# Kernel optimization log

Hardware: AMD Instinct MI355X
Metric: run time of the kernel (lower is better)

The kernel has to match this reference:

```python
import jax, jax.numpy as jnp
import numpy as np

A0 = 0.5291772105638411
KE = 14.399645351950548


def _softplus_inverse(x):
    return x + np.log(-np.expm1(-x))


def _sigma(x):
    # exp(-1/clamp(x,1e-12)) underflows to 0 for x<=0, so the where is nan-free
    return jnp.where(x > 0, jnp.exp(-1.0 / jnp.maximum(x, 1e-12)), 0.0)


def _switch(x, x_on, x_off):
    c = (x - x_on) / (x_off - x_on)
    s1 = _sigma(1.0 - c)
    s0 = _sigma(c)
    return s1 / (s1 + s0 + 1e-12)


def setup_inputs() -> dict:
    key = jax.random.key(0)
    k0, k1, k2, k3, k4 = jax.random.split(key, 5)
    N = 100000
    E = 6400000
    atomic_numbers = jax.random.uniform(k0, (N,), jnp.float32, 1.0, 30.0)
    cutoffs = jax.random.uniform(k1, (E, 1), jnp.float32)
    lengths = jax.random.uniform(k2, (E, 1), jnp.float32, 0.5, 3.0)
    senders = jax.random.randint(k3, (E,), 0, N)
    receivers = jax.random.randint(k4, (E,), 0, N)
    init = dict(a1=3.2, a2=0.9423, a3=0.4028, a4=0.2016,
                c1=0.1818, c2=0.5099, c3=0.2802, c4=0.02817,
                p=0.23, d=1.0 / (0.8854 * A0))
    params = {k + '_raw': jnp.asarray([_softplus_inverse(v)], jnp.float32)
              for k, v in init.items()}
    out = {'atomic_numbers': atomic_numbers, 'cutoffs': cutoffs,
           'senders': senders, 'receivers': receivers,
           'lengths': lengths, 'num_nodes': N}
    out.update(params)
    return out


def reference(atomic_numbers, cutoffs, senders, receivers, lengths, num_nodes,
              a1_raw, a2_raw, a3_raw, a4_raw,
              c1_raw, c2_raw, c3_raw, c4_raw, p_raw, d_raw):
    sp = jax.nn.softplus
    a1, a2, a3, a4 = sp(a1_raw), sp(a2_raw), sp(a3_raw), sp(a4_raw)
    c1, c2, c3, c4 = sp(c1_raw), sp(c2_raw), sp(c3_raw), sp(c4_raw)
    p, d = sp(p_raw), sp(d_raw)
    c_sum = c1 + c2 + c3 + c4
    c1, c2, c3, c4 = c1 / c_sum, c2 / c_sum, c3 / c_sum, c4 / c_sum

    cut = cutoffs[:, 0]   # [E]
    L = lengths[:, 0]     # [E]
    z_i = atomic_numbers[receivers]
    z_j = atomic_numbers[senders]

    x = KE * cut * (z_i * z_j) / jnp.maximum(L, 1e-6)
    rzd = L * (jnp.power(z_i, p) + jnp.power(z_j, p)) * d
    y = (c1 * jnp.exp(-a1 * rzd) + c2 * jnp.exp(-a2 * rzd)
         + c3 * jnp.exp(-a3 * rzd) + c4 * jnp.exp(-a4 * rzd))
    w = _switch(L, 0.0, 1.5)
    e_rep_edge = w * x * y * 0.5
    return jax.ops.segment_sum(e_rep_edge, receivers, num_segments=num_nodes)[:, None]
```

## Files before the change

kernel.cpp:

```cpp
#include <hip/hip_runtime.h>
#include <math.h>

#define C0KE 7.199822675975274f
#define LOG2E 1.4426950408889634f
#define BSHIFT 8
#define NBK 391
#define SLOTS 16
#define REG (NBK * SLOTS)
#define NBLK 1024
#define K1T 512
#define SENTINEL 0xFFFFFFFFu

__device__ __forceinline__ float softplusf(float x) {
    return (x > 20.0f) ? x : log1pf(__expf(x));
}

struct ZblParams { float A1, A2, A3, A4, c1, c2, c3, c4, p; };

__device__ __forceinline__ void load_params(
    const float* a1r, const float* a2r, const float* a3r, const float* a4r,
    const float* c1r, const float* c2r, const float* c3r, const float* c4r,
    const float* pr, const float* dr, ZblParams* P)
{
    float d  = softplusf(dr[0]);
    float s  = d * LOG2E;
    P->A1 = softplusf(a1r[0]) * s;
    P->A2 = softplusf(a2r[0]) * s;
    P->A3 = softplusf(a3r[0]) * s;
    P->A4 = softplusf(a4r[0]) * s;
    float c1 = softplusf(c1r[0]), c2 = softplusf(c2r[0]);
    float c3 = softplusf(c3r[0]), c4 = softplusf(c4r[0]);
    float inv = 1.0f / (c1 + c2 + c3 + c4);
    P->c1 = c1 * inv; P->c2 = c2 * inv; P->c3 = c3 * inv; P->c4 = c4 * inv;
    P->p = softplusf(pr[0]);
}

__device__ __forceinline__ float edge_energy_fast(
    float l, float cut_, float zi, float zj, const ZblParams& P)
{
    float c  = l * (1.0f / 1.5f);
    float om = 1.0f - c;
    float s1 = __builtin_amdgcn_exp2f(-LOG2E * __builtin_amdgcn_rcpf(om));
    float s0 = __builtin_amdgcn_exp2f(-LOG2E * __builtin_amdgcn_rcpf(c));
    float w  = s1 * __builtin_amdgcn_rcpf(s1 + s0);
    float x  = C0KE * cut_ * zi * zj * __builtin_amdgcn_rcpf(l);
    float S  = __builtin_amdgcn_exp2f(P.p * __builtin_amdgcn_logf(zi))
             + __builtin_amdgcn_exp2f(P.p * __builtin_amdgcn_logf(zj));
    float t  = l * S;
    float y  = P.c1 * __builtin_amdgcn_exp2f(-P.A1 * t)
             + P.c2 * __builtin_amdgcn_exp2f(-P.A2 * t)
             + P.c3 * __builtin_amdgcn_exp2f(-P.A3 * t)
             + P.c4 * __builtin_amdgcn_exp2f(-P.A4 * t);
    return w * x * y;
}

__global__ __launch_bounds__(K1T) void zbl_build(
    const float* __restrict__ z, const float* __restrict__ cut,
    const int* __restrict__ snd, const int* __restrict__ rcv,
    const float* __restrict__ len,
    const float* __restrict__ a1r, const float* __restrict__ a2r,
    const float* __restrict__ a3r, const float* __restrict__ a4r,
    const float* __restrict__ c1r, const float* __restrict__ c2r,
    const float* __restrict__ c3r, const float* __restrict__ c4r,
    const float* __restrict__ pr,  const float* __restrict__ dr,
    unsigned* __restrict__ Pg,
    float* __restrict__ out,
    int EPB, int E)
{
    __shared__ ZblParams P;
    __shared__ unsigned slots[REG];
    __shared__ unsigned fillc[NBK];

    const int tid = threadIdx.x;
    if (tid == 0)
        load_params(a1r, a2r, a3r, a4r, c1r, c2r, c3r, c4r, pr, dr, &P);
    for (int i = tid; i < REG; i += K1T) slots[i] = SENTINEL;
    for (int b = tid; b < NBK; b += K1T) fillc[b] = 0u;
    __syncthreads();
    const ZblParams Pl = P;

    const int blk = blockIdx.x;
    const int e0 = blk * EPB;
    const int e1 = min(e0 + EPB, E);
    const int nv = (e1 > e0) ? ((e1 - e0) >> 2) : 0;
    const int qb = e0 >> 2;
    const int etail = e0 + (nv << 2);
    const float4* Lq = (const float4*)len;
    const int4*   Rq = (const int4*)rcv;
    const float4* Cq = (const float4*)cut;
    const int4*   Sq = (const int4*)snd;

    for (int q = tid; q < nv; q += K1T) {
        float4 l4 = Lq[qb + q];
        if (l4.x < 1.5f || l4.y < 1.5f || l4.z < 1.5f || l4.w < 1.5f) {
            int4   r4 = Rq[qb + q];
            float4 c4 = Cq[qb + q];
            int4   s4 = Sq[qb + q];
            float Ls[4] = {l4.x, l4.y, l4.z, l4.w};
            float Cs[4] = {c4.x, c4.y, c4.z, c4.w};
            int   Ss[4] = {s4.x, s4.y, s4.z, s4.w};
            int   Rs[4] = {r4.x, r4.y, r4.z, r4.w};
            #pragma unroll
            for (int k = 0; k < 4; ++k) {
                if (Ls[k] < 1.5f) {
                    unsigned r = (unsigned)Rs[k];
                    float v = edge_energy_fast(Ls[k], Cs[k],
                                z[r], z[(unsigned)Ss[k]], Pl);
                    unsigned bk = r >> BSHIFT;
                    unsigned tk = atomicAdd(&fillc[bk], 1u);
                    if (tk < SLOTS) {
                        slots[bk * SLOTS + tk] =
                            (__float_as_uint(v) & 0xFFFFFF00u) | (r & 0xFFu);
                    } else {
                        unsafeAtomicAdd(&out[r], v);
                    }
                }
            }
        }
    }
    for (int e = etail + tid; e < e1; e += K1T) {
        float l = len[e];
        if (l < 1.5f) {
            unsigned r = (unsigned)rcv[e];
            float v = edge_energy_fast(l, cut[e], z[r], z[(unsigned)snd[e]], Pl);
            unsigned bk = r >> BSHIFT;
            unsigned tk = atomicAdd(&fillc[bk], 1u);
            if (tk < SLOTS)
                slots[bk * SLOTS + tk] =
                    (__float_as_uint(v) & 0xFFFFFF00u) | (r & 0xFFu);
            else
                unsafeAtomicAdd(&out[r], v);
        }
    }
    __syncthreads();

    unsigned base = (unsigned)blk * (unsigned)REG;
    for (int i = tid; i < REG; i += K1T)
        Pg[base + i] = slots[i];
}

__global__ __launch_bounds__(512) void zbl_reduce(
    const unsigned* __restrict__ Pg, float* __restrict__ out, int N)
{
    __shared__ float acc[256];
    const int tid = threadIdx.x;
    if (tid < 256) acc[tid] = 0.0f;
    __syncthreads();

    const int b = blockIdx.x;
    const uint4* Pq = (const uint4*)Pg;
    const int total = NBLK * (SLOTS / 4);
    for (int lin = tid; lin < total; lin += 512) {
        int r = lin >> 2, q = lin & 3;
        uint4 u = Pq[(size_t)r * (REG / 4) + (size_t)b * (SLOTS / 4) + q];
        if (u.x != SENTINEL)
            atomicAdd(&acc[u.x & 255u], __uint_as_float(u.x & 0xFFFFFF00u));
        if (u.y != SENTINEL)
            atomicAdd(&acc[u.y & 255u], __uint_as_float(u.y & 0xFFFFFF00u));
        if (u.z != SENTINEL)
            atomicAdd(&acc[u.z & 255u], __uint_as_float(u.z & 0xFFFFFF00u));
        if (u.w != SENTINEL)
            atomicAdd(&acc[u.w & 255u], __uint_as_float(u.w & 0xFFFFFF00u));
    }
    __syncthreads();

    int n = (b << BSHIFT) + tid;
    if (tid < 256 && n < N)
        out[n] += acc[tid];
}

__global__ __launch_bounds__(256) void zbl_direct(
    const float* __restrict__ z, const float* __restrict__ cut,
    const int* __restrict__ snd, const int* __restrict__ rcv,
    const float* __restrict__ len,
    const float* __restrict__ a1r, const float* __restrict__ a2r,
    const float* __restrict__ a3r, const float* __restrict__ a4r,
    const float* __restrict__ c1r, const float* __restrict__ c2r,
    const float* __restrict__ c3r, const float* __restrict__ c4r,
    const float* __restrict__ pr,  const float* __restrict__ dr,
    float* __restrict__ out, int n4, int E)
{
    __shared__ ZblParams P;
    if (threadIdx.x == 0)
        load_params(a1r, a2r, a3r, a4r, c1r, c2r, c3r, c4r, pr, dr, &P);
    __syncthreads();
    const ZblParams Pl = P;

    int i = blockIdx.x * blockDim.x + threadIdx.x;
    if (i >= n4) return;
    int base = i * 4;
    float cs[4], Ls[4]; int ss[4], rr[4]; int cnt;
    if (base + 4 <= E) {
        float4 c4v = ((const float4*)cut)[i];
        float4 l4v = ((const float4*)len)[i];
        int4   s4v = ((const int4*)snd)[i];
        int4   r4v = ((const int4*)rcv)[i];
        cs[0]=c4v.x; cs[1]=c4v.y; cs[2]=c4v.z; cs[3]=c4v.w;
        Ls[0]=l4v.x; Ls[1]=l4v.y; Ls[2]=l4v.z; Ls[3]=l4v.w;
        ss[0]=s4v.x; ss[1]=s4v.y; ss[2]=s4v.z; ss[3]=s4v.w;
        rr[0]=r4v.x; rr[1]=r4v.y; rr[2]=r4v.z; rr[3]=r4v.w;
        cnt = 4;
    } else {
        cnt = E - base;
        for (int k = 0; k < cnt; ++k) {
            cs[k] = cut[base+k]; Ls[k] = len[base+k];
            ss[k] = snd[base+k]; rr[k] = rcv[base+k];
        }
    }
    #pragma unroll
    for (int k = 0; k < 4; ++k) {
        if (k >= cnt) break;
        if (Ls[k] < 1.5f) {
            float e_rep = edge_energy_fast(Ls[k], cs[k], z[rr[k]], z[ss[k]], Pl);
            unsafeAtomicAdd(&out[rr[k]], e_rep);
        }
    }
}

extern "C" void kernel_launch(void* const* d_in, const int* in_sizes, int n_in,
                              void* d_out, int out_size, void* d_ws, size_t ws_size,
                              hipStream_t stream) {
    const float* z   = (const float*)d_in[0];
    const float* cut = (const float*)d_in[1];
    const int*   snd = (const int*)d_in[2];
    const int*   rcv = (const int*)d_in[3];
    const float* len = (const float*)d_in[4];
    const float* a1r = (const float*)d_in[6];
    const float* a2r = (const float*)d_in[7];
    const float* a3r = (const float*)d_in[8];
    const float* a4r = (const float*)d_in[9];
    const float* c1r = (const float*)d_in[10];
    const float* c2r = (const float*)d_in[11];
    const float* c3r = (const float*)d_in[12];
    const float* c4r = (const float*)d_in[13];
    const float* pr  = (const float*)d_in[14];
    const float* dr  = (const float*)d_in[15];

    float* out = (float*)d_out;
    int E = in_sizes[2];
    int N = out_size;

    size_t need1 = (size_t)NBLK * REG * sizeof(unsigned);

    hipMemsetAsync(d_out, 0, (size_t)N * sizeof(float), stream);

    if (ws_size >= need1) {
        int EPB = (((E + NBLK - 1) / NBLK) + 3) & ~3;
        unsigned* Pg = (unsigned*)d_ws;
        hipLaunchKernelGGL(zbl_build, dim3(NBLK), dim3(K1T), 0, stream,
                           z, cut, snd, rcv, len,
                           a1r, a2r, a3r, a4r, c1r, c2r, c3r, c4r, pr, dr,
                           Pg, out, EPB, E);
        hipLaunchKernelGGL(zbl_reduce, dim3(NBK), dim3(512), 0, stream,
                           (const unsigned*)Pg, out, N);
    } else {
        int n4 = (E + 3) / 4;
        int blocks = (n4 + 255) / 256;
        hipLaunchKernelGGL(zbl_direct, dim3(blocks), dim3(256), 0, stream,
                           z, cut, snd, rcv, len,
                           a1r, a2r, a3r, a4r, c1r, c2r, c3r, c4r, pr, dr,
                           out, n4, E);
    }
}
```

Before: 205.6 us.

## Prefetch next edge quad, batch z gathers, halve blocks, widen slot buffers

Software-pipelines the edge loop so each thread loads the next float4/int4 quad of lengths, receivers, cutoffs and senders while it processes the current one. It also issues all z gathers for a quad before computing energies, and loads all four arrays unconditionally instead of skipping them when no length passes the cutoff. Block count drops from 1024 to 512 with 20 slots per bucket, which shrinks the partial buffer the reduce kernel scans. Slot initialisation and write-back now use 128-bit vector stores. The trade-offs are more registers, extra bandwidth from the dropped length filter, and fewer blocks for parallelism and latency hiding.

```diff
diff --git a/kernel.cpp b/kernel.cpp
--- a/kernel.cpp
+++ b/kernel.cpp
@@ -5,9 +5,9 @@
 #define LOG2E 1.4426950408889634f
 #define BSHIFT 8
 #define NBK 391
-#define SLOTS 16
+#define SLOTS 20
 #define REG (NBK * SLOTS)
-#define NBLK 1024
+#define NBLK 512
 #define K1T 512
 #define SENTINEL 0xFFFFFFFFu
 
@@ -74,7 +74,11 @@
     const int tid = threadIdx.x;
     if (tid == 0)
         load_params(a1r, a2r, a3r, a4r, c1r, c2r, c3r, c4r, pr, dr, &P);
-    for (int i = tid; i < REG; i += K1T) slots[i] = SENTINEL;
+    {
+        uint4* s4p = (uint4*)slots;
+        const uint4 sent = make_uint4(SENTINEL, SENTINEL, SENTINEL, SENTINEL);
+        for (int i = tid; i < REG / 4; i += K1T) s4p[i] = sent;
+    }
     for (int b = tid; b < NBK; b += K1T) fillc[b] = 0u;
     __syncthreads();
     const ZblParams Pl = P;
@@ -90,22 +94,40 @@
     const float4* Cq = (const float4*)cut;
     const int4*   Sq = (const int4*)snd;
 
-    for (int q = tid; q < nv; q += K1T) {
-        float4 l4 = Lq[qb + q];
-        if (l4.x < 1.5f || l4.y < 1.5f || l4.z < 1.5f || l4.w < 1.5f) {
-            int4   r4 = Rq[qb + q];
-            float4 c4 = Cq[qb + q];
-            int4   s4 = Sq[qb + q];
+    const int trips = (nv + K1T - 1) / K1T;
+    int rel = tid;
+    int qi  = qb + tid;
+    bool have = rel < nv;
+    float4 l4, c4; int4 r4, s4;
+    if (have) { l4 = Lq[qi]; r4 = Rq[qi]; c4 = Cq[qi]; s4 = Sq[qi]; }
+
+    for (int it = 0; it < trips; ++it) {
+        const int reln = rel + K1T;
+        const int qin  = qi + K1T;
+        const bool haveN = reln < nv;
+        float4 l4n, c4n; int4 r4n, s4n;
+        if (haveN) { l4n = Lq[qin]; r4n = Rq[qin]; c4n = Cq[qin]; s4n = Sq[qin]; }
+
+        if (have) {
             float Ls[4] = {l4.x, l4.y, l4.z, l4.w};
             float Cs[4] = {c4.x, c4.y, c4.z, c4.w};
             int   Ss[4] = {s4.x, s4.y, s4.z, s4.w};
             int   Rs[4] = {r4.x, r4.y, r4.z, r4.w};
+            bool  pass[4];
+            float zi[4], zj[4];
             #pragma unroll
             for (int k = 0; k < 4; ++k) {
-                if (Ls[k] < 1.5f) {
-                    unsigned r = (unsigned)Rs[k];
-                    float v = edge_energy_fast(Ls[k], Cs[k],
-                                z[r], z[(unsigned)Ss[k]], Pl);
+                pass[k] = Ls[k] < 1.5f;
+                if (pass[k]) {
+                    zi[k] = z[(unsigned)Rs[k]];
+                    zj[k] = z[(unsigned)Ss[k]];
+                }
+            }
+            #pragma unroll
+            for (int k = 0; k < 4; ++k) {
+                if (pass[k]) {
+                    float v = edge_energy_fast(Ls[k], Cs[k], zi[k], zj[k], Pl);
+                    unsigned r  = (unsigned)Rs[k];
                     unsigned bk = r >> BSHIFT;
                     unsigned tk = atomicAdd(&fillc[bk], 1u);
                     if (tk < SLOTS) {
@@ -117,7 +139,10 @@
                 }
             }
         }
-    }
+        l4 = l4n; c4 = c4n; r4 = r4n; s4 = s4n;
+        rel = reln; qi = qin; have = haveN;
+    }
+
     for (int e = etail + tid; e < e1; e += K1T) {
         float l = len[e];
         if (l < 1.5f) {
@@ -134,9 +159,11 @@
     }
     __syncthreads();
 
-    unsigned base = (unsigned)blk * (unsigned)REG;
-    for (int i = tid; i < REG; i += K1T)
-        Pg[base + i] = slots[i];
+    {
+        uint4* dst = (uint4*)(Pg + (size_t)blk * REG);
+        const uint4* src = (const uint4*)slots;
+        for (int i = tid; i < REG / 4; i += K1T) dst[i] = src[i];
+    }
 }
 
 __global__ __launch_bounds__(512) void zbl_reduce(
@@ -151,7 +178,8 @@
     const uint4* Pq = (const uint4*)Pg;
     const int total = NBLK * (SLOTS / 4);
     for (int lin = tid; lin < total; lin += 512) {
-        int r = lin >> 2, q = lin & 3;
+        int r = lin / (SLOTS / 4);
+        int q = lin - r * (SLOTS / 4);
         uint4 u = Pq[(size_t)r * (REG / 4) + (size_t)b * (SLOTS / 4) + q];
         if (u.x != SENTINEL)
             atomicAdd(&acc[u.x & 255u], __uint_as_float(u.x & 0xFFFFFF00u));
```

Result: faster. 198.2 us (-3.6%).

## Replace shared-memory slot binning with replicated global atomic accumulation arrays

Applied to the files above, without the earlier changes.

Drops the per-block LDS slot-binning build and the reduce pass that scanned every block's slots. Edges now go straight to global atomic adds on one of 16 replicated output arrays, chosen by block index, and a merge kernel then sums the replicas into the output. This removes the large partial-slot workspace writes and the reduce scan, and spreads atomic contention across the replicas. The cost is clearing and reading 16×N floats and more global atomics, because every surviving edge now does one instead of only the overflow edges.

```diff
diff --git a/kernel.cpp b/kernel.cpp
--- a/kernel.cpp
+++ b/kernel.cpp
@@ -3,13 +3,8 @@
 
 #define C0KE 7.199822675975274f
 #define LOG2E 1.4426950408889634f
-#define BSHIFT 8
-#define NBK 391
-#define SLOTS 16
-#define REG (NBK * SLOTS)
-#define NBLK 1024
-#define K1T 512
-#define SENTINEL 0xFFFFFFFFu
+#define RREP 16
+#define SCT 256
 
 __device__ __forceinline__ float softplusf(float x) {
     return (x > 20.0f) ? x : log1pf(__expf(x));
@@ -54,7 +49,7 @@
     return w * x * y;
 }
 
-__global__ __launch_bounds__(K1T) void zbl_build(
+__global__ __launch_bounds__(SCT) void zbl_scatter(
     const float* __restrict__ z, const float* __restrict__ cut,
     const int* __restrict__ snd, const int* __restrict__ rcv,
     const float* __restrict__ len,
@@ -63,110 +58,84 @@
     const float* __restrict__ c1r, const float* __restrict__ c2r,
     const float* __restrict__ c3r, const float* __restrict__ c4r,
     const float* __restrict__ pr,  const float* __restrict__ dr,
-    unsigned* __restrict__ Pg,
-    float* __restrict__ out,
-    int EPB, int E)
+    float* __restrict__ ws,
+    int nq, int E, int N)
 {
     __shared__ ZblParams P;
-    __shared__ unsigned slots[REG];
-    __shared__ unsigned fillc[NBK];
-
-    const int tid = threadIdx.x;
-    if (tid == 0)
+    if (threadIdx.x == 0)
         load_params(a1r, a2r, a3r, a4r, c1r, c2r, c3r, c4r, pr, dr, &P);
-    for (int i = tid; i < REG; i += K1T) slots[i] = SENTINEL;
-    for (int b = tid; b < NBK; b += K1T) fillc[b] = 0u;
     __syncthreads();
     const ZblParams Pl = P;
 
-    const int blk = blockIdx.x;
-    const int e0 = blk * EPB;
-    const int e1 = min(e0 + EPB, E);
-    const int nv = (e1 > e0) ? ((e1 - e0) >> 2) : 0;
-    const int qb = e0 >> 2;
-    const int etail = e0 + (nv << 2);
-    const float4* Lq = (const float4*)len;
-    const int4*   Rq = (const int4*)rcv;
-    const float4* Cq = (const float4*)cut;
-    const int4*   Sq = (const int4*)snd;
-
-    for (int q = tid; q < nv; q += K1T) {
-        float4 l4 = Lq[qb + q];
-        if (l4.x < 1.5f || l4.y < 1.5f || l4.z < 1.5f || l4.w < 1.5f) {
-            int4   r4 = Rq[qb + q];
-            float4 c4 = Cq[qb + q];
-            int4   s4 = Sq[qb + q];
-            float Ls[4] = {l4.x, l4.y, l4.z, l4.w};
-            float Cs[4] = {c4.x, c4.y, c4.z, c4.w};
-            int   Ss[4] = {s4.x, s4.y, s4.z, s4.w};
-            int   Rs[4] = {r4.x, r4.y, r4.z, r4.w};
+    float* __restrict__ rw = ws + (size_t)(blockIdx.x & (RREP - 1)) * (size_t)N;
+
+    int i = blockIdx.x * SCT + threadIdx.x;
+    if (i >= nq) return;
+    int base = i << 2;
+
+    float Ls[4], Cs[4]; int Ss[4], Rs[4]; int cnt;
+    if (base + 4 <= E) {
+        float4 l4 = ((const float4*)len)[i];
+        int4   r4 = ((const int4*)rcv)[i];
+        float4 c4 = ((const float4*)cut)[i];
+        int4   s4 = ((const int4*)snd)[i];
+        Ls[0]=l4.x; Ls[1]=l4.y; Ls[2]=l4.z; Ls[3]=l4.w;
+        Cs[0]=c4.x; Cs[1]=c4.y; Cs[2]=c4.z; Cs[3]=c4.w;
+        Ss[0]=s4.x; Ss[1]=s4.y; Ss[2]=s4.z; Ss[3]=s4.w;
+        Rs[0]=r4.x; Rs[1]=r4.y; Rs[2]=r4.z; Rs[3]=r4.w;
+        cnt = 4;
+    } else {
+        cnt = E - base;
+        for (int k = 0; k < cnt; ++k) {
+            Ls[k] = len[base+k]; Cs[k] = cut[base+k];
+            Ss[k] = snd[base+k]; Rs[k] = rcv[base+k];
+        }
+    }
+
+    bool pass[4]; float zi[4], zj[4];
+    #pragma unroll
+    for (int k = 0; k < 4; ++k) {
+        pass[k] = (k < cnt) && (Ls[k] < 1.5f);
+        if (pass[k]) {
+            zi[k] = z[(unsigned)Rs[k]];
+            zj[k] = z[(unsigned)Ss[k]];
+        }
+    }
+    #pragma unroll
+    for (int k = 0; k < 4; ++k) {
+        if (pass[k]) {
+            float v = edge_energy_fast(Ls[k], Cs[k], zi[k], zj[k], Pl);
+            unsafeAtomicAdd(&rw[(unsigned)Rs[k]], v);
+        }
+    }
+}
+
+__global__ __launch_bounds__(256) void zbl_merge(
+    const float* __restrict__ ws, float* __restrict__ out, int N)
+{
+    const int idx = blockIdx.x * 256 + threadIdx.x;
+    const int stride = gridDim.x * 256;
+    if ((N & 3) == 0) {
+        const int n4 = N >> 2;
+        const float4* w4 = (const float4*)ws;
+        float4* o4 = (float4*)out;
+        for (int i = idx; i < n4; i += stride) {
+            float4 s = w4[i];
             #pragma unroll
-            for (int k = 0; k < 4; ++k) {
-                if (Ls[k] < 1.5f) {
-                    unsigned r = (unsigned)Rs[k];
-                    float v = edge_energy_fast(Ls[k], Cs[k],
-                                z[r], z[(unsigned)Ss[k]], Pl);
-                    unsigned bk = r >> BSHIFT;
-                    unsigned tk = atomicAdd(&fillc[bk], 1u);
-                    if (tk < SLOTS) {
-                        slots[bk * SLOTS + tk] =
-                            (__float_as_uint(v) & 0xFFFFFF00u) | (r & 0xFFu);
-                    } else {
-                        unsafeAtomicAdd(&out[r], v);
-                    }
-                }
+            for (int r = 1; r < RREP; ++r) {
+                float4 t = w4[(size_t)r * n4 + i];
+                s.x += t.x; s.y += t.y; s.z += t.z; s.w += t.w;
             }
-        }
-    }
-    for (int e = etail + tid; e < e1; e += K1T) {
-        float l = len[e];
-        if (l < 1.5f) {
-            unsigned r = (unsigned)rcv[e];
-            float v = edge_energy_fast(l, cut[e], z[r], z[(unsigned)snd[e]], Pl);
-            unsigned bk = r >> BSHIFT;
-            unsigned tk = atomicAdd(&fillc[bk], 1u);
-            if (tk < SLOTS)
-                slots[bk * SLOTS + tk] =
-                    (__float_as_uint(v) & 0xFFFFFF00u) | (r & 0xFFu);
-            else
-                unsafeAtomicAdd(&out[r], v);
-        }
-    }
-    __syncthreads();
-
-    unsigned base = (unsigned)blk * (unsigned)REG;
-    for (int i = tid; i < REG; i += K1T)
-        Pg[base + i] = slots[i];
-}
-
-__global__ __launch_bounds__(512) void zbl_reduce(
-    const unsigned* __restrict__ Pg, float* __restrict__ out, int N)
-{
-    __shared__ float acc[256];
-    const int tid = threadIdx.x;
-    if (tid < 256) acc[tid] = 0.0f;
-    __syncthreads();
-
-    const int b = blockIdx.x;
-    const uint4* Pq = (const uint4*)Pg;
-    const int total = NBLK * (SLOTS / 4);
-    for (int lin = tid; lin < total; lin += 512) {
-        int r = lin >> 2, q = lin & 3;
-        uint4 u = Pq[(size_t)r * (REG / 4) + (size_t)b * (SLOTS / 4) + q];
-        if (u.x != SENTINEL)
-            atomicAdd(&acc[u.x & 255u], __uint_as_float(u.x & 0xFFFFFF00u));
-        if (u.y != SENTINEL)
-            atomicAdd(&acc[u.y & 255u], __uint_as_float(u.y & 0xFFFFFF00u));
-        if (u.z != SENTINEL)
-            atomicAdd(&acc[u.z & 255u], __uint_as_float(u.z & 0xFFFFFF00u));
-        if (u.w != SENTINEL)
-            atomicAdd(&acc[u.w & 255u], __uint_as_float(u.w & 0xFFFFFF00u));
-    }
-    __syncthreads();
-
-    int n = (b << BSHIFT) + tid;
-    if (tid < 256 && n < N)
-        out[n] += acc[tid];
+            o4[i] = s;
+        }
+    } else {
+        for (int n = idx; n < N; n += stride) {
+            float s = 0.0f;
+            #pragma unroll
+            for (int r = 0; r < RREP; ++r) s += ws[(size_t)r * N + n];
+            out[n] = s;
+        }
+    }
 }
 
 __global__ __launch_bounds__(256) void zbl_direct(
@@ -240,20 +209,21 @@
     int E = in_sizes[2];
     int N = out_size;
 
-    size_t need1 = (size_t)NBLK * REG * sizeof(unsigned);
-
-    hipMemsetAsync(d_out, 0, (size_t)N * sizeof(float), stream);
-
-    if (ws_size >= need1) {
-        int EPB = (((E + NBLK - 1) / NBLK) + 3) & ~3;
-        unsigned* Pg = (unsigned*)d_ws;
-        hipLaunchKernelGGL(zbl_build, dim3(NBLK), dim3(K1T), 0, stream,
+    size_t needR = (size_t)RREP * (size_t)N * sizeof(float);
+
+    if (ws_size >= needR) {
+        float* ws = (float*)d_ws;
+        hipMemsetAsync(ws, 0, needR, stream);
+        int nq = (E + 3) / 4;
+        int blocks = (nq + SCT - 1) / SCT;
+        hipLaunchKernelGGL(zbl_scatter, dim3(blocks), dim3(SCT), 0, stream,
                            z, cut, snd, rcv, len,
                            a1r, a2r, a3r, a4r, c1r, c2r, c3r, c4r, pr, dr,
-                           Pg, out, EPB, E);
-        hipLaunchKernelGGL(zbl_reduce, dim3(NBK), dim3(512), 0, stream,
-                           (const unsigned*)Pg, out, N);
-    } else {
+                           ws, nq, E, N);
+        hipLaunchKernelGGL(zbl_merge, dim3(128), dim3(256), 0, stream,
+                           (const float*)ws, out, N);
+    } else {
+        hipMemsetAsync(d_out, 0, (size_t)N * sizeof(float), stream);
         int n4 = (E + 3) / 4;
         int blocks = (n4 + 255) / 256;
         hipLaunchKernelGGL(zbl_direct, dim3(blocks), dim3(256), 0, stream,
```

New measurement: 264.0 us. +28.4%, slower.
